# Optimization experiments

Measured on AMD Instinct MI355X. Metric: run time of the kernel, lower is better.

## Reference

```python
import jax, jax.numpy as jnp
import numpy as np

CAPACITY = 1024


def setup_inputs() -> dict:
    T, H, I, E, K = 2048, 1024, 1408, 8, 2
    key = jax.random.key(0)
    k0, k1, k2, k3, k4 = jax.random.split(key, 5)
    hidden_states = jax.random.normal(k0, (T, H), dtype=jnp.float32)
    w1 = jax.random.normal(k1, (E, 2 * I, H), dtype=jnp.float32) * 0.02  # [gate; up]
    w2 = jax.random.normal(k2, (E, H, I), dtype=jnp.float32) * 0.02
    topk_weights = jax.random.uniform(k3, (T, K), dtype=jnp.float32)
    topk_ids = jax.random.randint(k4, (T, K), 0, E, dtype=jnp.int32)
    return {"hidden_states": hidden_states, "w1": w1, "w2": w2,
            "topk_weights": topk_weights, "topk_ids": topk_ids}


def reference(hidden_states, w1, w2, topk_weights, topk_ids):
    # MoE: prepare(dispatch) -> grouped expert GEMM (silu-gated MLP) -> finalize(combine)
    T, H = hidden_states.shape
    E = w1.shape[0]
    I = w2.shape[2]
    K = topk_ids.shape[1]
    C = CAPACITY

    # ---- prepare: dispatch token copies to per-expert buffers ----
    flat_ids = topk_ids.reshape(-1)                       # (T*K,)
    onehot = jax.nn.one_hot(flat_ids, E, dtype=jnp.int32)  # (T*K, E)
    cs = jnp.cumsum(onehot, axis=0)                        # running per-expert counts
    pos = jnp.take_along_axis(cs, flat_ids[:, None], axis=1)[:, 0] - 1  # slot in expert buffer
    keep = pos < C
    pos_c = jnp.where(keep, pos, 0)

    x_flat = jnp.repeat(hidden_states, K, axis=0)          # (T*K, H)
    x_e = jnp.zeros((E, C, H), dtype=hidden_states.dtype)
    x_e = x_e.at[flat_ids, pos_c].add(jnp.where(keep[:, None], x_flat, 0.0))

    # ---- grouped expert GEMM: silu(gate) * up, then down-proj ----
    h = jnp.einsum('ech,eoh->eco', x_e, w1)                # (E, C, 2I)
    gate, up = h[..., :I], h[..., I:]
    act = jax.nn.silu(gate) * up                           # (E, C, I)
    y = jnp.einsum('eci,ehi->ech', act, w2)                # (E, C, H)

    # ---- finalize: gather back, apply router weights, reduce over top-k ----
    y_flat = y[flat_ids, pos_c] * (keep[:, None].astype(y.dtype)) \
             * topk_weights.reshape(-1, 1)                 # (T*K, H)
    out = y_flat.reshape(T, K, H).sum(axis=1)              # (T, H)
    return out.astype(hidden_states.dtype)
```

## Files before the change

kernel.cpp:

```cpp
#include <hip/hip_runtime.h>

#define NE 8
#define CAP 1024
#define HD 1024
#define ID 1408
#define TT 2048

typedef __attribute__((ext_vector_type(8))) short bf16x8;
typedef __attribute__((ext_vector_type(4))) float f32x4;
typedef unsigned short u16;
typedef unsigned int u32;
typedef unsigned long long u64;

__device__ __forceinline__ u16 f2bf(float f) {
  u32 u = __float_as_uint(f);
  u = (u + 0x7fffu + ((u >> 16) & 1u)) >> 16;
  return (u16)u;
}
__device__ __forceinline__ float bf2f(u16 b) {
  return __uint_as_float(((u32)b) << 16);
}

__device__ __forceinline__ void async_cp16(const void* g, void* l) {
  __builtin_amdgcn_global_load_lds(
      (const __attribute__((address_space(1))) u32*)g,
      (__attribute__((address_space(3))) u32*)l, 16, 0, 0);
}

__global__ void cvt_kernel(const float4* __restrict__ src, ushort4* __restrict__ dst, int n4) {
  int i = blockIdx.x * 256 + threadIdx.x;
  if (i >= n4) return;
  float4 v = src[i];
  ushort4 o;
  o.x = f2bf(v.x); o.y = f2bf(v.y); o.z = f2bf(v.z); o.w = f2bf(v.w);
  dst[i] = o;
}

__global__ void cvt_w1_kernel(const float4* __restrict__ src, ushort4* __restrict__ dst) {
  int n = blockIdx.x;
  int e = blockIdx.y;
  int tid = threadIdx.x;
  int np = (n < ID) ? (2 * n) : (2 * (n - ID) + 1);
  float4 v = src[((size_t)e * 2 * ID + n) * (HD / 4) + tid];
  ushort4 o;
  o.x = f2bf(v.x); o.y = f2bf(v.y); o.z = f2bf(v.z); o.w = f2bf(v.w);
  dst[((size_t)e * 2 * ID + np) * (HD / 4) + tid] = o;
}

__global__ void zero_kernel(float4* __restrict__ out, int n4) {
  int i = blockIdx.x * 256 + threadIdx.x;
  if (i < n4) out[i] = float4{0.f, 0.f, 0.f, 0.f};
}

__global__ void route_kernel(const int* __restrict__ ids, int* __restrict__ rowmap,
                             int* __restrict__ flatpos, int* __restrict__ counts) {
  __shared__ int ids_s[TT * 2];
  __shared__ int sc[256][NE + 1];
  int tid = threadIdx.x;
  for (int i = tid; i < TT * 2; i += 256) ids_s[i] = ids[i];
  __syncthreads();
  int base = tid * 16;
  u64 own64 = 0;
#pragma unroll
  for (int j = 0; j < 16; ++j) own64 += 1ull << (ids_s[base + j] * 8);
  int own[NE];
#pragma unroll
  for (int e = 0; e < NE; ++e) { own[e] = (int)((own64 >> (e * 8)) & 0xff); sc[tid][e] = own[e]; }
  __syncthreads();
  for (int off = 1; off < 256; off <<= 1) {
    int v[NE];
    if (tid >= off) {
#pragma unroll
      for (int e = 0; e < NE; ++e) v[e] = sc[tid - off][e];
    }
    __syncthreads();
    if (tid >= off) {
#pragma unroll
      for (int e = 0; e < NE; ++e) sc[tid][e] += v[e];
    }
    __syncthreads();
  }
  if (tid == 255) {
#pragma unroll
    for (int e = 0; e < NE; ++e) counts[e] = sc[255][e] < CAP ? sc[255][e] : CAP;
  }
  int excl[NE];
#pragma unroll
  for (int e = 0; e < NE; ++e) excl[e] = sc[tid][e] - own[e];
  __syncthreads();
#pragma unroll
  for (int e = 0; e < NE; ++e) sc[tid][e] = excl[e];
#pragma unroll
  for (int j = 0; j < 16; ++j) {
    int f = base + j;
    int e = ids_s[f];
    int p = sc[tid][e]++;
    if (p < CAP) { rowmap[e * CAP + p] = f; flatpos[f] = p; }
    else flatpos[f] = -1;
  }
}

__global__ __launch_bounds__(256) void gemm1_kernel(
    const u16* __restrict__ A, const u16* __restrict__ B, u16* __restrict__ Hb,
    const int* __restrict__ rowmap, const int* __restrict__ counts) {
  int e = blockIdx.x;
  int count = counts[e];
  int m0 = blockIdx.y * 128;
  if (m0 >= count) return;
  int n0 = blockIdx.z * 128;
  int tid = threadIdx.x;
  int lane = tid & 63, wid = tid >> 6;
  int wm = wid >> 1, wn = wid & 1;
  int q = lane >> 4, lm = lane & 15;

  __shared__ __align__(16) char smA[128 * 128];
  __shared__ __align__(16) char smB[128 * 128];

  int rloc = tid >> 3;
  int chs = ((tid & 7) ^ (rloc & 7)) * 8;
  const u16* aP[4];
  const u16* bP[4];
#pragma unroll
  for (int i = 0; i < 4; ++i) {
    int row = rloc + 32 * i;
    int gr = m0 + row;
    int f = (gr < count) ? rowmap[e * CAP + gr] : 0;
    aP[i] = A + (size_t)(f >> 1) * HD + chs;
    bP[i] = B + ((size_t)e * 2 * ID + n0 + row) * HD + chs;
  }

  f32x4 zero = {0.f, 0.f, 0.f, 0.f};
  f32x4 acc[4][4];
#pragma unroll
  for (int mi = 0; mi < 4; ++mi)
#pragma unroll
    for (int ni = 0; ni < 4; ++ni) acc[mi][ni] = zero;

  for (int kt = 0; kt < HD / 64; ++kt) {
    int ko = kt * 64;
#pragma unroll
    for (int i = 0; i < 4; ++i) {
      async_cp16(aP[i] + ko, smA + (i * 256 + tid) * 16);
      async_cp16(bP[i] + ko, smB + (i * 256 + tid) * 16);
    }
    asm volatile("s_waitcnt vmcnt(0)" ::: "memory");
    __syncthreads();
#pragma unroll
    for (int s = 0; s < 2; ++s) {
      bf16x8 af[4], bfr[4];
#pragma unroll
      for (int mi = 0; mi < 4; ++mi) {
        int row = wm * 64 + mi * 16 + lm;
        af[mi] = *(const bf16x8*)(smA + row * 128 + (((s * 4 + q) ^ (lm & 7)) * 16));
      }
#pragma unroll
      for (int ni = 0; ni < 4; ++ni) {
        int row = wn * 64 + ni * 16 + lm;
        bfr[ni] = *(const bf16x8*)(smB + row * 128 + (((s * 4 + q) ^ (lm & 7)) * 16));
      }
#pragma unroll
      for (int mi = 0; mi < 4; ++mi)
#pragma unroll
        for (int ni = 0; ni < 4; ++ni)
          acc[mi][ni] = __builtin_amdgcn_mfma_f32_16x16x32_bf16(af[mi], bfr[ni], acc[mi][ni], 0, 0, 0);
    }
    __syncthreads();
  }

  bool isGate = (lm & 1) == 0;
#pragma unroll
  for (int mi = 0; mi < 4; ++mi) {
#pragma unroll
    for (int ni = 0; ni < 4; ++ni) {
      int cOut = (n0 >> 1) + wn * 32 + ni * 8 + (lm >> 1);
#pragma unroll
      for (int r = 0; r < 4; ++r) {
        float v = acc[mi][ni][r];
        float partner = __shfl_xor(v, 1, 64);
        if (isGate) {
          float g = v, u = partner;
          float a = g / (1.f + __expf(-g)) * u;
          int row = m0 + wm * 64 + mi * 16 + q * 4 + r;
          Hb[((size_t)e * CAP + row) * ID + cOut] = f2bf(a);
        }
      }
    }
  }
}

__global__ __launch_bounds__(256) void gemm2_kernel(
    const u16* __restrict__ A, const u16* __restrict__ B, float* __restrict__ out,
    const int* __restrict__ rowmap, const int* __restrict__ counts,
    const float* __restrict__ tw) {
  int e = blockIdx.x;
  int count = counts[e];
  int m0 = blockIdx.y * 64;
  if (m0 >= count) return;
  int n0 = blockIdx.z * 128;
  int tid = threadIdx.x;
  int lane = tid & 63, wid = tid >> 6;
  int wm = wid >> 1, wn = wid & 1;
  int q = lane >> 4, lm = lane & 15;

  __shared__ __align__(16) char smA[64 * 128];
  __shared__ __align__(16) char smB[128 * 128];

  int rloc = tid >> 3;
  int chs = ((tid & 7) ^ (rloc & 7)) * 8;
  const u16* aP[2];
  const u16* bP[4];
#pragma unroll
  for (int i = 0; i < 2; ++i)
    aP[i] = A + ((size_t)e * CAP + m0 + rloc + 32 * i) * ID + chs;
#pragma unroll
  for (int i = 0; i < 4; ++i)
    bP[i] = B + ((size_t)e * HD + n0 + rloc + 32 * i) * ID + chs;

  f32x4 zero = {0.f, 0.f, 0.f, 0.f};
  f32x4 acc[2][4];
#pragma unroll
  for (int mi = 0; mi < 2; ++mi)
#pragma unroll
    for (int ni = 0; ni < 4; ++ni) acc[mi][ni] = zero;

  for (int kt = 0; kt < ID / 64; ++kt) {
    int ko = kt * 64;
#pragma unroll
    for (int i = 0; i < 2; ++i)
      async_cp16(aP[i] + ko, smA + (i * 256 + tid) * 16);
#pragma unroll
    for (int i = 0; i < 4; ++i)
      async_cp16(bP[i] + ko, smB + (i * 256 + tid) * 16);
    asm volatile("s_waitcnt vmcnt(0)" ::: "memory");
    __syncthreads();
#pragma unroll
    for (int s = 0; s < 2; ++s) {
      bf16x8 af[2], bfr[4];
#pragma unroll
      for (int mi = 0; mi < 2; ++mi) {
        int row = wm * 32 + mi * 16 + lm;
        af[mi] = *(const bf16x8*)(smA + row * 128 + (((s * 4 + q) ^ (lm & 7)) * 16));
      }
#pragma unroll
      for (int ni = 0; ni < 4; ++ni) {
        int row = wn * 64 + ni * 16 + lm;
        bfr[ni] = *(const bf16x8*)(smB + row * 128 + (((s * 4 + q) ^ (lm & 7)) * 16));
      }
#pragma unroll
      for (int mi = 0; mi < 2; ++mi)
#pragma unroll
        for (int ni = 0; ni < 4; ++ni)
          acc[mi][ni] = __builtin_amdgcn_mfma_f32_16x16x32_bf16(af[mi], bfr[ni], acc[mi][ni], 0, 0, 0);
    }
    __syncthreads();
  }

#pragma unroll
  for (int mi = 0; mi < 2; ++mi) {
#pragma unroll
    for (int r = 0; r < 4; ++r) {
      int grow = m0 + wm * 32 + mi * 16 + q * 4 + r;
      if (grow < count) {
        int f = rowmap[e * CAP + grow];
        float w = tw[f];
        int t = f >> 1;
#pragma unroll
        for (int ni = 0; ni < 4; ++ni) {
          int col = n0 + wn * 64 + ni * 16 + lm;
          atomicAdd(&out[(size_t)t * HD + col], w * acc[mi][ni][r]);
        }
      }
    }
  }
}

extern "C" void kernel_launch(void* const* d_in, const int* in_sizes, int n_in,
                              void* d_out, int out_size, void* d_ws, size_t ws_size,
                              hipStream_t stream) {
  const float* hidden = (const float*)d_in[0];
  const float* w1 = (const float*)d_in[1];
  const float* w2 = (const float*)d_in[2];
  const float* tw = (const float*)d_in[3];
  const int* ids = (const int*)d_in[4];
  float* out = (float*)d_out;

  char* p = (char*)d_ws;
  auto alloc = [&](size_t b) { char* r = p; p += (b + 255) & ~(size_t)255; return r; };
  u16* bw1 = (u16*)alloc((size_t)NE * 2 * ID * HD * 2);
  u16* bw2 = (u16*)alloc((size_t)NE * HD * ID * 2);
  u16* bx = (u16*)alloc((size_t)TT * HD * 2);
  u16* hbuf = (u16*)alloc((size_t)NE * CAP * ID * 2);
  int* rowmap = (int*)alloc((size_t)NE * CAP * 4);
  int* flatpos = (int*)alloc((size_t)TT * 2 * 4);
  int* counts = (int*)alloc((size_t)NE * 4);

  cvt_w1_kernel<<<dim3(2 * ID, NE), 256, 0, stream>>>((const float4*)w1, (ushort4*)bw1);
  int n4w2 = NE * HD * ID / 4;
  cvt_kernel<<<(n4w2 + 255) / 256, 256, 0, stream>>>((const float4*)w2, (ushort4*)bw2, n4w2);
  int n4x = TT * HD / 4;
  cvt_kernel<<<(n4x + 255) / 256, 256, 0, stream>>>((const float4*)hidden, (ushort4*)bx, n4x);

  route_kernel<<<1, 256, 0, stream>>>(ids, rowmap, flatpos, counts);

  int n4o = TT * HD / 4;
  zero_kernel<<<(n4o + 255) / 256, 256, 0, stream>>>((float4*)out, n4o);

  gemm1_kernel<<<dim3(NE, CAP / 128, 2 * ID / 128), 256, 0, stream>>>(
      bx, bw1, hbuf, rowmap, counts);

  gemm2_kernel<<<dim3(NE, CAP / 64, HD / 128), 256, 0, stream>>>(
      hbuf, bw2, out, rowmap, counts, tw);
}
```

Baseline: 292.3 us.

## Shrink GEMM tiles, regroup gate/up interleave, and stage activation stores via LDS

Converted w1 rows are now interleaved in 16-row gate/up blocks rather than alternating rows. This lets each lane compute silu(gate)*up from its own accumulators without a cross-lane shuffle. Gemm1 is cut to 64-row M tiles and gemm2 to 64-column N tiles, which raises block count and occupancy on a GPU with many CUs. The gemm1 epilogue writes the activations to LDS first and then issues coalesced 16-byte global stores. The cost is lower arithmetic intensity per block and more reloading of the weight tiles.

```diff
diff --git a/kernel.cpp b/kernel.cpp
--- a/kernel.cpp
+++ b/kernel.cpp
@@ -40,7 +40,8 @@
   int n = blockIdx.x;
   int e = blockIdx.y;
   int tid = threadIdx.x;
-  int np = (n < ID) ? (2 * n) : (2 * (n - ID) + 1);
+  int j = (n < ID) ? n : (n - ID);
+  int np = (j >> 4) * 32 + (j & 15) + ((n < ID) ? 0 : 16);
   float4 v = src[((size_t)e * 2 * ID + n) * (HD / 4) + tid];
   ushort4 o;
   o.x = f2bf(v.x); o.y = f2bf(v.y); o.z = f2bf(v.z); o.w = f2bf(v.w);
@@ -105,7 +106,7 @@
     const int* __restrict__ rowmap, const int* __restrict__ counts) {
   int e = blockIdx.x;
   int count = counts[e];
-  int m0 = blockIdx.y * 128;
+  int m0 = blockIdx.y * 64;
   if (m0 >= count) return;
   int n0 = blockIdx.z * 128;
   int tid = threadIdx.x;
@@ -113,44 +114,46 @@
   int wm = wid >> 1, wn = wid & 1;
   int q = lane >> 4, lm = lane & 15;
 
-  __shared__ __align__(16) char smA[128 * 128];
+  __shared__ __align__(16) char smA[64 * 128];
   __shared__ __align__(16) char smB[128 * 128];
 
   int rloc = tid >> 3;
   int chs = ((tid & 7) ^ (rloc & 7)) * 8;
-  const u16* aP[4];
+  const u16* aP[2];
   const u16* bP[4];
 #pragma unroll
-  for (int i = 0; i < 4; ++i) {
-    int row = rloc + 32 * i;
-    int gr = m0 + row;
+  for (int i = 0; i < 2; ++i) {
+    int gr = m0 + rloc + 32 * i;
     int f = (gr < count) ? rowmap[e * CAP + gr] : 0;
     aP[i] = A + (size_t)(f >> 1) * HD + chs;
-    bP[i] = B + ((size_t)e * 2 * ID + n0 + row) * HD + chs;
-  }
+  }
+#pragma unroll
+  for (int i = 0; i < 4; ++i)
+    bP[i] = B + ((size_t)e * 2 * ID + n0 + rloc + 32 * i) * HD + chs;
 
   f32x4 zero = {0.f, 0.f, 0.f, 0.f};
-  f32x4 acc[4][4];
-#pragma unroll
-  for (int mi = 0; mi < 4; ++mi)
+  f32x4 acc[2][4];
+#pragma unroll
+  for (int mi = 0; mi < 2; ++mi)
 #pragma unroll
     for (int ni = 0; ni < 4; ++ni) acc[mi][ni] = zero;
 
   for (int kt = 0; kt < HD / 64; ++kt) {
     int ko = kt * 64;
 #pragma unroll
-    for (int i = 0; i < 4; ++i) {
+    for (int i = 0; i < 2; ++i)
       async_cp16(aP[i] + ko, smA + (i * 256 + tid) * 16);
+#pragma unroll
+    for (int i = 0; i < 4; ++i)
       async_cp16(bP[i] + ko, smB + (i * 256 + tid) * 16);
-    }
     asm volatile("s_waitcnt vmcnt(0)" ::: "memory");
     __syncthreads();
 #pragma unroll
     for (int s = 0; s < 2; ++s) {
-      bf16x8 af[4], bfr[4];
-#pragma unroll
-      for (int mi = 0; mi < 4; ++mi) {
-        int row = wm * 64 + mi * 16 + lm;
+      bf16x8 af[2], bfr[4];
+#pragma unroll
+      for (int mi = 0; mi < 2; ++mi) {
+        int row = wm * 32 + mi * 16 + lm;
         af[mi] = *(const bf16x8*)(smA + row * 128 + (((s * 4 + q) ^ (lm & 7)) * 16));
       }
 #pragma unroll
@@ -159,7 +162,7 @@
         bfr[ni] = *(const bf16x8*)(smB + row * 128 + (((s * 4 + q) ^ (lm & 7)) * 16));
       }
 #pragma unroll
-      for (int mi = 0; mi < 4; ++mi)
+      for (int mi = 0; mi < 2; ++mi)
 #pragma unroll
         for (int ni = 0; ni < 4; ++ni)
           acc[mi][ni] = __builtin_amdgcn_mfma_f32_16x16x32_bf16(af[mi], bfr[ni], acc[mi][ni], 0, 0, 0);
@@ -167,24 +170,31 @@
     __syncthreads();
   }
 
-  bool isGate = (lm & 1) == 0;
-#pragma unroll
-  for (int mi = 0; mi < 4; ++mi) {
-#pragma unroll
-    for (int ni = 0; ni < 4; ++ni) {
-      int cOut = (n0 >> 1) + wn * 32 + ni * 8 + (lm >> 1);
+  u16* smOut = (u16*)smB;
+#pragma unroll
+  for (int mi = 0; mi < 2; ++mi) {
+#pragma unroll
+    for (int k = 0; k < 2; ++k) {
+      int colL = wn * 32 + k * 16 + lm;
 #pragma unroll
       for (int r = 0; r < 4; ++r) {
-        float v = acc[mi][ni][r];
-        float partner = __shfl_xor(v, 1, 64);
-        if (isGate) {
-          float g = v, u = partner;
-          float a = g / (1.f + __expf(-g)) * u;
-          int row = m0 + wm * 64 + mi * 16 + q * 4 + r;
-          Hb[((size_t)e * CAP + row) * ID + cOut] = f2bf(a);
-        }
-      }
-    }
+        float g = acc[mi][2 * k][r];
+        float u = acc[mi][2 * k + 1][r];
+        float a = g / (1.f + __expf(-g)) * u;
+        int row = wm * 32 + mi * 16 + q * 4 + r;
+        smOut[row * 72 + colL] = f2bf(a);
+      }
+    }
+  }
+  __syncthreads();
+  {
+    int row = tid >> 2, seg = tid & 3;
+    const u16* sp = smOut + row * 72 + seg * 16;
+    bf16x8 v0 = *(const bf16x8*)sp;
+    bf16x8 v1 = *(const bf16x8*)(sp + 8);
+    u16* dp = Hb + ((size_t)e * CAP + m0 + row) * ID + (n0 >> 1) + seg * 16;
+    *(bf16x8*)dp = v0;
+    *(bf16x8*)(dp + 8) = v1;
   }
 }
 
@@ -196,60 +206,58 @@
   int count = counts[e];
   int m0 = blockIdx.y * 64;
   if (m0 >= count) return;
-  int n0 = blockIdx.z * 128;
+  int n0 = blockIdx.z * 64;
   int tid = threadIdx.x;
   int lane = tid & 63, wid = tid >> 6;
   int wm = wid >> 1, wn = wid & 1;
   int q = lane >> 4, lm = lane & 15;
 
   __shared__ __align__(16) char smA[64 * 128];
-  __shared__ __align__(16) char smB[128 * 128];
+  __shared__ __align__(16) char smB[64 * 128];
 
   int rloc = tid >> 3;
   int chs = ((tid & 7) ^ (rloc & 7)) * 8;
   const u16* aP[2];
-  const u16* bP[4];
-#pragma unroll
-  for (int i = 0; i < 2; ++i)
+  const u16* bP[2];
+#pragma unroll
+  for (int i = 0; i < 2; ++i) {
     aP[i] = A + ((size_t)e * CAP + m0 + rloc + 32 * i) * ID + chs;
-#pragma unroll
-  for (int i = 0; i < 4; ++i)
     bP[i] = B + ((size_t)e * HD + n0 + rloc + 32 * i) * ID + chs;
+  }
 
   f32x4 zero = {0.f, 0.f, 0.f, 0.f};
-  f32x4 acc[2][4];
+  f32x4 acc[2][2];
 #pragma unroll
   for (int mi = 0; mi < 2; ++mi)
 #pragma unroll
-    for (int ni = 0; ni < 4; ++ni) acc[mi][ni] = zero;
+    for (int ni = 0; ni < 2; ++ni) acc[mi][ni] = zero;
 
   for (int kt = 0; kt < ID / 64; ++kt) {
     int ko = kt * 64;
 #pragma unroll
-    for (int i = 0; i < 2; ++i)
+    for (int i = 0; i < 2; ++i) {
       async_cp16(aP[i] + ko, smA + (i * 256 + tid) * 16);
-#pragma unroll
-    for (int i = 0; i < 4; ++i)
       async_cp16(bP[i] + ko, smB + (i * 256 + tid) * 16);
+    }
     asm volatile("s_waitcnt vmcnt(0)" ::: "memory");
     __syncthreads();
 #pragma unroll
     for (int s = 0; s < 2; ++s) {
-      bf16x8 af[2], bfr[4];
+      bf16x8 af[2], bfr[2];
 #pragma unroll
       for (int mi = 0; mi < 2; ++mi) {
         int row = wm * 32 + mi * 16 + lm;
         af[mi] = *(const bf16x8*)(smA + row * 128 + (((s * 4 + q) ^ (lm & 7)) * 16));
       }
 #pragma unroll
-      for (int ni = 0; ni < 4; ++ni) {
-        int row = wn * 64 + ni * 16 + lm;
+      for (int ni = 0; ni < 2; ++ni) {
+        int row = wn * 32 + ni * 16 + lm;
         bfr[ni] = *(const bf16x8*)(smB + row * 128 + (((s * 4 + q) ^ (lm & 7)) * 16));
       }
 #pragma unroll
       for (int mi = 0; mi < 2; ++mi)
 #pragma unroll
-        for (int ni = 0; ni < 4; ++ni)
+        for (int ni = 0; ni < 2; ++ni)
           acc[mi][ni] = __builtin_amdgcn_mfma_f32_16x16x32_bf16(af[mi], bfr[ni], acc[mi][ni], 0, 0, 0);
     }
     __syncthreads();
@@ -265,8 +273,8 @@
         float w = tw[f];
         int t = f >> 1;
 #pragma unroll
-        for (int ni = 0; ni < 4; ++ni) {
-          int col = n0 + wn * 64 + ni * 16 + lm;
+        for (int ni = 0; ni < 2; ++ni) {
+          int col = n0 + wn * 32 + ni * 16 + lm;
           atomicAdd(&out[(size_t)t * HD + col], w * acc[mi][ni][r]);
         }
       }
@@ -305,9 +313,9 @@
   int n4o = TT * HD / 4;
   zero_kernel<<<(n4o + 255) / 256, 256, 0, stream>>>((float4*)out, n4o);
 
-  gemm1_kernel<<<dim3(NE, CAP / 128, 2 * ID / 128), 256, 0, stream>>>(
+  gemm1_kernel<<<dim3(NE, CAP / 64, 2 * ID / 128), 256, 0, stream>>>(
       bx, bw1, hbuf, rowmap, counts);
 
-  gemm2_kernel<<<dim3(NE, CAP / 64, HD / 128), 256, 0, stream>>>(
+  gemm2_kernel<<<dim3(NE, CAP / 64, HD / 64), 256, 0, stream>>>(
       hbuf, bw2, out, rowmap, counts, tw);
 }
```

Result: faster. 271.3 us (-7.2%).
